# Kernel tuning notes

Measured on AMD Instinct MI355X. Metric: run time of the kernel, lower is better.

## Reference

```python
import jax, jax.numpy as jnp
import numpy as np

D_MODEL = 1024
N_HEADS = 16
HEAD_DIM = D_MODEL // N_HEADS


def apply_rope(x):
    # x: [B, S, H, Dh]; standard rotate-half RoPE over head_dim
    B, S, H, Dh = x.shape
    inv_freq = 1.0 / (10000.0 ** (jnp.arange(0, Dh, 2, dtype=jnp.float32) / Dh))  # [Dh/2]
    pos = jnp.arange(S, dtype=jnp.float32)
    freqs = pos[:, None] * inv_freq[None, :]          # [S, Dh/2]
    cos = jnp.cos(freqs)[None, :, None, :]            # [1, S, 1, Dh/2]
    sin = jnp.sin(freqs)[None, :, None, :]
    x1, x2 = x[..., :Dh // 2], x[..., Dh // 2:]
    return jnp.concatenate([x1 * cos - x2 * sin, x1 * sin + x2 * cos], axis=-1)


def setup_inputs() -> dict:
    key = jax.random.key(0)
    ks = jax.random.split(key, 8)
    B, S, D = 2, 2048, D_MODEL
    s = 0.02
    return {
        "query": jax.random.normal(ks[0], (B, S, D), dtype=jnp.float32),
        "key": jax.random.normal(ks[1], (B, S, D), dtype=jnp.float32),
        "value": jax.random.normal(ks[2], (B, S, D), dtype=jnp.float32),
        "Wq": jax.random.normal(ks[3], (D, D), dtype=jnp.float32) * s,
        "Wk": jax.random.normal(ks[4], (D, D), dtype=jnp.float32) * s,
        "Wv": jax.random.normal(ks[5], (D, D), dtype=jnp.float32) * s,
        "Wo": jax.random.normal(ks[6], (D, D), dtype=jnp.float32) * s,
        "bo": jax.random.normal(ks[7], (D,), dtype=jnp.float32) * s,
    }


def reference(query, key, value, Wq, Wk, Wv, Wo, bo):
    B, Sq, D = query.shape
    Skv = key.shape[1]
    H, Dh = N_HEADS, HEAD_DIM
    scale = Dh ** -0.5
    # projections (torch Linear: x @ W.T)
    q = (query @ Wq.T).reshape(B, Sq, H, Dh)
    k = (key @ Wk.T).reshape(B, Skv, H, Dh)
    v = (value @ Wv.T).reshape(B, Skv, H, Dh)
    q = apply_rope(q)
    k = apply_rope(k)
    # scores: [B, H, Sq, Skv]
    scores = jnp.einsum("bqhd,bkhd->bhqk", q, k) * scale
    attn_weights = jax.nn.softmax(scores, axis=-1)
    out = jnp.einsum("bhqk,bkhd->bqhd", attn_weights, v).reshape(B, Sq, D)
    out = out @ Wo.T + bo
    return out, attn_weights
```

## Files before the change

kernel.cpp:

```cpp
#include <hip/hip_runtime.h>
#include <math.h>

#define D_MODEL 1024
#define SEQ     2048
#define NB      2
#define NH      16
#define DH      64
#define ROWS    (NB*SEQ)
#define OUT_ELEMS ((size_t)ROWS*D_MODEL)

typedef short bf16x8 __attribute__((ext_vector_type(8)));
typedef short bf16x4 __attribute__((ext_vector_type(4)));
typedef float f32x4  __attribute__((ext_vector_type(4)));

#define AS1 __attribute__((address_space(1)))
#define AS3 __attribute__((address_space(3)))

__device__ __forceinline__ float bf2f(short u){
    union{float f; unsigned v;} x; x.v = ((unsigned)(unsigned short)u) << 16; return x.f;
}
__device__ __forceinline__ short f2bf(float f){
    union{float f; unsigned v;} x; x.f = f;
    unsigned r = (x.v + 0x7FFF + ((x.v >> 16) & 1)) >> 16;
    return (short)r;
}
__device__ __forceinline__ int swz8(int row, int slot){ return slot ^ ((row + (row>>3)) & 7); }

#define MFMA16(a,b,c) __builtin_amdgcn_mfma_f32_16x16x32_bf16((a),(b),(c),0,0,0)

#define EXPSC 0.18033688011112042f

__global__ __launch_bounds__(256) void prep(const float* __restrict__ Wq,
                                            const float* __restrict__ Wk,
                                            const float* __restrict__ Wv,
                                            const float* __restrict__ Wo,
                                            const float* __restrict__ qx,
                                            const float* __restrict__ kx,
                                            const float* __restrict__ vx,
                                            short* __restrict__ wqkv,
                                            short* __restrict__ wob,
                                            short* __restrict__ xb,
                                            float* __restrict__ tab)
{
    int i = blockIdx.x*256 + threadIdx.x;
    if (i < 1048576) {
        int sel = i >> 18;
        int loc = i & 262143;
        const float* src = sel==0 ? Wq : sel==1 ? Wk : sel==2 ? Wv : Wo;
        short* dst = sel < 3 ? wqkv + (size_t)sel*1048576 : wob;
        float4 v = *(const float4*)&src[(size_t)loc*4];
        bf16x4 o = { f2bf(v.x), f2bf(v.y), f2bf(v.z), f2bf(v.w) };
        *(bf16x4*)&dst[(size_t)loc*4] = o;
    } else if (i < 4194304) {
        int e = i - 1048576;
        int sel = e >> 20;
        int loc = e & 1048575;
        const float* src = sel==0 ? qx : sel==1 ? kx : vx;
        short* dst = xb + (size_t)sel*OUT_ELEMS;
        float4 v = *(const float4*)&src[(size_t)loc*4];
        bf16x4 o = { f2bf(v.x), f2bf(v.y), f2bf(v.z), f2bf(v.w) };
        *(bf16x4*)&dst[(size_t)loc*4] = o;
    } else {
        int e = i - 4194304;
        int j = e & 31, s = e >> 5;
        float ang = (float)s * exp2f(-(float)j * 0.41524101186092437f);
        float sn, cs; sincosf(ang, &sn, &cs);
        tab[(size_t)s*64 + j*2]     = cs;
        tab[(size_t)s*64 + j*2 + 1] = sn;
    }
}

__global__ __launch_bounds__(256) void gemm_qkv(const short* __restrict__ xb,
                                                const short* __restrict__ wqkv,
                                                const float* __restrict__ tab,
                                                short* __restrict__ qb,
                                                short* __restrict__ kb,
                                                short* __restrict__ vbt)
{
    const int z = blockIdx.z;
    const short* A = xb + (size_t)z*OUT_ELEMS;
    const short* B = wqkv + (size_t)z*D_MODEL*D_MODEL;

    __shared__ __align__(16) short Alds[128*64];
    __shared__ __align__(16) short Blds[128*64];
    const int t = threadIdx.x, lane = t & 63, wid = t >> 6;
    const int m0 = blockIdx.y << 7, n0 = blockIdx.x << 7;
    const int wm = (wid >> 1) << 6, wn = (wid & 1) << 6;
    const int l15 = lane & 15, l4 = lane >> 4;
    const int gchunk = (lane & 7) ^ (lane >> 3);
    const int rxor = l15 & 7;

    f32x4 acc[4][4] = {};

    for (int k0 = 0; k0 < D_MODEL; k0 += 64) {
        __syncthreads();
        #pragma unroll
        for (int u = 0; u < 4; ++u) {
            int row = u*32 + wid*8 + (lane >> 3);
            const short* ga = &A[(size_t)(m0 + row)*D_MODEL + k0 + gchunk*8];
            const short* gb = &B[(size_t)(n0 + row)*D_MODEL + k0 + gchunk*8];
            __builtin_amdgcn_global_load_lds((const AS1 unsigned*)ga,
                (AS3 unsigned*)&Alds[u*2048 + wid*512], 16, 0, 0);
            __builtin_amdgcn_global_load_lds((const AS1 unsigned*)gb,
                (AS3 unsigned*)&Blds[u*2048 + wid*512], 16, 0, 0);
        }
        __syncthreads();
        #pragma unroll
        for (int kk = 0; kk < 2; ++kk) {
            bf16x8 af[4], bfr[4];
            #pragma unroll
            for (int mf = 0; mf < 4; ++mf)
                af[mf] = *(const bf16x8*)&Alds[(wm + mf*16 + l15)*64
                                               + ((kk*4 + l4) ^ rxor)*8];
            #pragma unroll
            for (int nf = 0; nf < 4; ++nf)
                bfr[nf] = *(const bf16x8*)&Blds[(wn + nf*16 + l15)*64
                                                + ((kk*4 + l4) ^ rxor)*8];
            #pragma unroll
            for (int mf = 0; mf < 4; ++mf)
                #pragma unroll
                for (int nf = 0; nf < 4; ++nf)
                    acc[mf][nf] = MFMA16(af[mf], bfr[nf], acc[mf][nf]);
        }
    }

    if (z < 2) {
        short* C = z==0 ? qb : kb;
        #pragma unroll
        for (int mf = 0; mf < 4; ++mf)
            #pragma unroll
            for (int j = 0; j < 4; ++j) {
                int row = m0 + wm + mf*16 + l4*4 + j;
                int s = row & (SEQ-1);
                #pragma unroll
                for (int p = 0; p < 2; ++p) {
                    int d31 = p*16 + l15;
                    float2 cs2 = *(const float2*)&tab[(size_t)s*64 + d31*2];
                    float x1 = acc[mf][p][j], x2 = acc[mf][p+2][j];
                    size_t rb = (size_t)row*D_MODEL + n0 + wn;
                    C[rb + p*16 + l15]       = f2bf(x1*cs2.x - x2*cs2.y);
                    C[rb + (p+2)*16 + l15]   = f2bf(x1*cs2.y + x2*cs2.x);
                }
            }
    } else {
        #pragma unroll
        for (int nf = 0; nf < 4; ++nf) {
            int col = n0 + wn + nf*16 + l15;
            int hh = col >> 6, d = col & 63;
            #pragma unroll
            for (int mf = 0; mf < 4; ++mf)
                #pragma unroll
                for (int j = 0; j < 4; ++j) {
                    int row = m0 + wm + mf*16 + l4*4 + j;
                    int b = row >> 11, s = row & (SEQ-1);
                    vbt[(((size_t)(b*NH + hh))*DH + d)*SEQ + s] = f2bf(acc[mf][nf][j]);
                }
        }
    }
}

__global__ __launch_bounds__(256) void gemm_out(const short* __restrict__ A,
                                                const short* __restrict__ B,
                                                const float* __restrict__ bias,
                                                float* __restrict__ Cout)
{
    __shared__ __align__(16) short Alds[128*64];
    __shared__ __align__(16) short Blds[128*64];
    const int t = threadIdx.x, lane = t & 63, wid = t >> 6;
    const int m0 = blockIdx.y << 7, n0 = blockIdx.x << 7;
    const int wm = (wid >> 1) << 6, wn = (wid & 1) << 6;
    const int l15 = lane & 15, l4 = lane >> 4;
    const int gchunk = (lane & 7) ^ (lane >> 3);
    const int rxor = l15 & 7;

    f32x4 acc[4][4] = {};

    for (int k0 = 0; k0 < D_MODEL; k0 += 64) {
        __syncthreads();
        #pragma unroll
        for (int u = 0; u < 4; ++u) {
            int row = u*32 + wid*8 + (lane >> 3);
            const short* ga = &A[(size_t)(m0 + row)*D_MODEL + k0 + gchunk*8];
            const short* gb = &B[(size_t)(n0 + row)*D_MODEL + k0 + gchunk*8];
            __builtin_amdgcn_global_load_lds((const AS1 unsigned*)ga,
                (AS3 unsigned*)&Alds[u*2048 + wid*512], 16, 0, 0);
            __builtin_amdgcn_global_load_lds((const AS1 unsigned*)gb,
                (AS3 unsigned*)&Blds[u*2048 + wid*512], 16, 0, 0);
        }
        __syncthreads();
        #pragma unroll
        for (int kk = 0; kk < 2; ++kk) {
            bf16x8 af[4], bfr[4];
            #pragma unroll
            for (int mf = 0; mf < 4; ++mf)
                af[mf] = *(const bf16x8*)&Alds[(wm + mf*16 + l15)*64
                                               + ((kk*4 + l4) ^ rxor)*8];
            #pragma unroll
            for (int nf = 0; nf < 4; ++nf)
                bfr[nf] = *(const bf16x8*)&Blds[(wn + nf*16 + l15)*64
                                                + ((kk*4 + l4) ^ rxor)*8];
            #pragma unroll
            for (int mf = 0; mf < 4; ++mf)
                #pragma unroll
                for (int nf = 0; nf < 4; ++nf)
                    acc[mf][nf] = MFMA16(af[mf], bfr[nf], acc[mf][nf]);
        }
    }

    #pragma unroll
    for (int nf = 0; nf < 4; ++nf) {
        int col = n0 + wn + nf*16 + l15;
        float bv = bias[col];
        #pragma unroll
        for (int mf = 0; mf < 4; ++mf)
            #pragma unroll
            for (int j = 0; j < 4; ++j) {
                int row = m0 + wm + mf*16 + l4*4 + j;
                Cout[(size_t)row*D_MODEL + col] = acc[mf][nf][j] + bv;
            }
    }
}

__global__ __launch_bounds__(512) void attn_fused(const short* __restrict__ qb,
                                                  const short* __restrict__ kb,
                                                  const short* __restrict__ vbt,
                                                  float* __restrict__ attn,
                                                  short* __restrict__ aob)
{
    __shared__ __align__(16) short Klds[2][64*64];
    __shared__ __align__(16) short Vt  [2][64*64];
    __shared__ __align__(16) short Plds[8*16*64];
    const int t = threadIdx.x, lane = t & 63, wv = t >> 6;
    const int bid = blockIdx.x;
    const int nb = (bid & 7)*64 + (bid >> 3);
    const int rb = nb & 15, bh = nb >> 4;
    const int h = bh & 15;
    const size_t bs0 = (size_t)(bh >> 4) * SEQ;
    const int qrow0 = rb << 7;
    const int l15 = lane & 15, l4 = lane >> 4;
    const int srow = t >> 3, ssl = t & 7;
    const int soff = srow*64 + swz8(srow, ssl)*8;

    bf16x8 qf[2];
    {
        int qrow = qrow0 + wv*16 + l15;
        const short* qp = &qb[(bs0 + qrow)*D_MODEL + h*DH + l4*8];
        qf[0] = *(const bf16x8*)&qp[0];
        qf[1] = *(const bf16x8*)&qp[32];
    }

    const short* kbase  = &kb[(bs0 + srow)*D_MODEL + h*DH + ssl*8];
    const short* vtbase = &vbt[((size_t)bh*DH + srow)*SEQ + ssl*8];

    float lsum = 0.f;
    {
        bf16x8 kreg = *(const bf16x8*)&kbase[0];
        *(bf16x8*)&Klds[0][soff] = kreg;
        kreg = *(const bf16x8*)&kbase[(size_t)64*D_MODEL];
        __syncthreads();
        int cur = 0;
        for (int kt = 0; kt < SEQ; kt += 64, cur ^= 1) {
            if (kt + 64 < SEQ) {
                *(bf16x8*)&Klds[cur^1][soff] = kreg;
                if (kt + 128 < SEQ)
                    kreg = *(const bf16x8*)&kbase[(size_t)(kt+128)*D_MODEL];
            }
            f32x4 sc[4] = {};
            __builtin_amdgcn_s_setprio(1);
            #pragma unroll
            for (int kk = 0; kk < 2; ++kk)
                #pragma unroll
                for (int nf = 0; nf < 4; ++nf) {
                    int krow = nf*16 + l15;
                    bf16x8 kf = *(const bf16x8*)&Klds[cur][krow*64 + swz8(krow, kk*4 + l4)*8];
                    sc[nf] = MFMA16(kf, qf[kk], sc[nf]);
                }
            __builtin_amdgcn_s_setprio(0);
            #pragma unroll
            for (int nf = 0; nf < 4; ++nf)
                #pragma unroll
                for (int j = 0; j < 4; ++j)
                    lsum += exp2f(sc[nf][j]*EXPSC);
            __syncthreads();
        }
    }
    lsum += __shfl_xor(lsum, 16);
    lsum += __shfl_xor(lsum, 32);
    const float li = 1.0f / lsum;

    f32x4 o[4] = {};
    const size_t wrow = ((size_t)bh*SEQ + qrow0 + wv*16 + l15)*SEQ;
    short* pbase = &Plds[wv*1024 + l15*64];
    {
        bf16x8 kreg = *(const bf16x8*)&kbase[0];
        bf16x8 vreg = *(const bf16x8*)&vtbase[0];
        *(bf16x8*)&Klds[0][soff] = kreg;
        *(bf16x8*)&Vt  [0][soff] = vreg;
        kreg = *(const bf16x8*)&kbase[(size_t)64*D_MODEL];
        vreg = *(const bf16x8*)&vtbase[64];
        __syncthreads();
        int cur = 0;
        for (int kt = 0; kt < SEQ; kt += 64, cur ^= 1) {
            if (kt + 64 < SEQ) {
                *(bf16x8*)&Klds[cur^1][soff] = kreg;
                *(bf16x8*)&Vt  [cur^1][soff] = vreg;
                if (kt + 128 < SEQ) {
                    kreg = *(const bf16x8*)&kbase[(size_t)(kt+128)*D_MODEL];
                    vreg = *(const bf16x8*)&vtbase[kt+128];
                }
            }
            f32x4 sc[4] = {};
            __builtin_amdgcn_s_setprio(1);
            #pragma unroll
            for (int kk = 0; kk < 2; ++kk)
                #pragma unroll
                for (int nf = 0; nf < 4; ++nf) {
                    int krow = nf*16 + l15;
                    bf16x8 kf = *(const bf16x8*)&Klds[cur][krow*64 + swz8(krow, kk*4 + l4)*8];
                    sc[nf] = MFMA16(kf, qf[kk], sc[nf]);
                }
            __builtin_amdgcn_s_setprio(0);
            #pragma unroll
            for (int nf = 0; nf < 4; ++nf) {
                float w0 = exp2f(sc[nf][0]*EXPSC) * li;
                float w1 = exp2f(sc[nf][1]*EXPSC) * li;
                float w2 = exp2f(sc[nf][2]*EXPSC) * li;
                float w3 = exp2f(sc[nf][3]*EXPSC) * li;
                f32x4 wv4 = { w0, w1, w2, w3 };
                __builtin_nontemporal_store(wv4,
                    (f32x4*)&attn[wrow + kt + nf*16 + l4*4]);
                bf16x4 pw = { f2bf(w0), f2bf(w1), f2bf(w2), f2bf(w3) };
                *(bf16x4*)&pbase[swz8(l15, nf*2 + (l4>>1))*8 + (l4&1)*4] = pw;
            }
            __builtin_amdgcn_s_setprio(1);
            #pragma unroll
            for (int kk = 0; kk < 2; ++kk) {
                bf16x8 pa = *(const bf16x8*)&pbase[swz8(l15, kk*4 + l4)*8];
                #pragma unroll
                for (int nf = 0; nf < 4; ++nf) {
                    int d = nf*16 + l15;
                    bf16x8 vf = *(const bf16x8*)&Vt[cur][d*64 + swz8(d, kk*4 + l4)*8];
                    o[nf] = MFMA16(pa, vf, o[nf]);
                }
            }
            __builtin_amdgcn_s_setprio(0);
            __syncthreads();
        }
    }
    #pragma unroll
    for (int nf = 0; nf < 4; ++nf)
        #pragma unroll
        for (int j = 0; j < 4; ++j) {
            int qr = qrow0 + wv*16 + l4*4 + j;
            aob[(bs0 + qr)*D_MODEL + h*DH + nf*16 + l15] = f2bf(o[nf][j]);
        }
}

extern "C" void kernel_launch(void* const* d_in, const int* in_sizes, int n_in,
                              void* d_out, int out_size, void* d_ws, size_t ws_size,
                              hipStream_t stream)
{
    const float* query = (const float*)d_in[0];
    const float* key_  = (const float*)d_in[1];
    const float* value = (const float*)d_in[2];
    const float* Wq    = (const float*)d_in[3];
    const float* Wk    = (const float*)d_in[4];
    const float* Wv    = (const float*)d_in[5];
    const float* Wo    = (const float*)d_in[6];
    const float* bo    = (const float*)d_in[7];

    float* out  = (float*)d_out;
    float* attn = out + OUT_ELEMS;
    short* xb   = (short*)attn;

    short* wqkv = (short*)d_ws;
    short* wob  = wqkv + (size_t)3*1048576;
    short* qb   = wob  + (size_t)1048576;
    short* kb   = qb + OUT_ELEMS;
    short* vbt  = kb + OUT_ELEMS;
    short* aob  = vbt + OUT_ELEMS;
    float* tab  = (float*)(aob + OUT_ELEMS);

    dim3 blk(256);

    hipLaunchKernelGGL(prep, dim3(16640), blk, 0, stream,
                       Wq, Wk, Wv, Wo, query, key_, value, wqkv, wob, xb, tab);
    hipLaunchKernelGGL(gemm_qkv, dim3(8, 32, 3), blk, 0, stream,
                       xb, wqkv, tab, qb, kb, vbt);
    hipLaunchKernelGGL(attn_fused, dim3(512), dim3(512), 0, stream,
                       qb, kb, vbt, attn, aob);
    hipLaunchKernelGGL(gemm_out, dim3(8, 32), blk, 0, stream, aob, wob, bo, out);
}
```

Measured before the change: 291.8 us.

## Process two 16-row query subtiles per wave in attention with 256-thread blocks

The attention kernel now runs 4 waves of 256 threads instead of 8 waves, and each wave handles 32 query rows as two 16-row subtiles. Each K and V fragment read from LDS then feeds two MFMAs, halving LDS fragment reads per unit of work and giving each thread two tile rows to load. The cost is higher register pressure and fewer waves per block to hide the latency of the large attention-weight store stream.

Result: slower. 309.6 us (+6.1%).

```diff
diff --git a/kernel.cpp b/kernel.cpp
--- a/kernel.cpp
+++ b/kernel.cpp
@@ -221,7 +221,7 @@
     }
 }
 
-__global__ __launch_bounds__(512) void attn_fused(const short* __restrict__ qb,
+__global__ __launch_bounds__(256) void attn_fused(const short* __restrict__ qb,
                                                   const short* __restrict__ kb,
                                                   const short* __restrict__ vbt,
                                                   float* __restrict__ attn,
@@ -229,7 +229,7 @@
 {
     __shared__ __align__(16) short Klds[2][64*64];
     __shared__ __align__(16) short Vt  [2][64*64];
-    __shared__ __align__(16) short Plds[8*16*64];
+    __shared__ __align__(16) short Plds[4*2*16*64];
     const int t = threadIdx.x, lane = t & 63, wv = t >> 6;
     const int bid = blockIdx.x;
     const int nb = (bid & 7)*64 + (bid >> 3);
@@ -238,34 +238,44 @@
     const size_t bs0 = (size_t)(bh >> 4) * SEQ;
     const int qrow0 = rb << 7;
     const int l15 = lane & 15, l4 = lane >> 4;
-    const int srow = t >> 3, ssl = t & 7;
-    const int soff = srow*64 + swz8(srow, ssl)*8;
-
-    bf16x8 qf[2];
+    const int sr0 = t >> 3, ssl = t & 7;
+    const int soff0 = sr0*64 + swz8(sr0, ssl)*8;
+    const int soff1 = (sr0+32)*64 + swz8(sr0+32, ssl)*8;
+
+    bf16x8 qf[2][2];
+    #pragma unroll
+    for (int sub = 0; sub < 2; ++sub) {
+        int qrow = qrow0 + wv*32 + sub*16 + l15;
+        const short* qp = &qb[(bs0 + qrow)*D_MODEL + h*DH + l4*8];
+        qf[sub][0] = *(const bf16x8*)&qp[0];
+        qf[sub][1] = *(const bf16x8*)&qp[32];
+    }
+
+    const short* kbase0  = &kb[(bs0 + sr0)*D_MODEL + h*DH + ssl*8];
+    const short* kbase1  = &kb[(bs0 + sr0 + 32)*D_MODEL + h*DH + ssl*8];
+    const short* vtbase0 = &vbt[((size_t)bh*DH + sr0)*SEQ + ssl*8];
+    const short* vtbase1 = &vbt[((size_t)bh*DH + sr0 + 32)*SEQ + ssl*8];
+
+    float lsum0 = 0.f, lsum1 = 0.f;
     {
-        int qrow = qrow0 + wv*16 + l15;
-        const short* qp = &qb[(bs0 + qrow)*D_MODEL + h*DH + l4*8];
-        qf[0] = *(const bf16x8*)&qp[0];
-        qf[1] = *(const bf16x8*)&qp[32];
-    }
-
-    const short* kbase  = &kb[(bs0 + srow)*D_MODEL + h*DH + ssl*8];
-    const short* vtbase = &vbt[((size_t)bh*DH + srow)*SEQ + ssl*8];
-
-    float lsum = 0.f;
-    {
-        bf16x8 kreg = *(const bf16x8*)&kbase[0];
-        *(bf16x8*)&Klds[0][soff] = kreg;
-        kreg = *(const bf16x8*)&kbase[(size_t)64*D_MODEL];
+        bf16x8 kr0 = *(const bf16x8*)&kbase0[0];
+        bf16x8 kr1 = *(const bf16x8*)&kbase1[0];
+        *(bf16x8*)&Klds[0][soff0] = kr0;
+        *(bf16x8*)&Klds[0][soff1] = kr1;
+        kr0 = *(const bf16x8*)&kbase0[(size_t)64*D_MODEL];
+        kr1 = *(const bf16x8*)&kbase1[(size_t)64*D_MODEL];
         __syncthreads();
         int cur = 0;
         for (int kt = 0; kt < SEQ; kt += 64, cur ^= 1) {
             if (kt + 64 < SEQ) {
-                *(bf16x8*)&Klds[cur^1][soff] = kreg;
-                if (kt + 128 < SEQ)
-                    kreg = *(const bf16x8*)&kbase[(size_t)(kt+128)*D_MODEL];
-            }
-            f32x4 sc[4] = {};
+                *(bf16x8*)&Klds[cur^1][soff0] = kr0;
+                *(bf16x8*)&Klds[cur^1][soff1] = kr1;
+                if (kt + 128 < SEQ) {
+                    kr0 = *(const bf16x8*)&kbase0[(size_t)(kt+128)*D_MODEL];
+                    kr1 = *(const bf16x8*)&kbase1[(size_t)(kt+128)*D_MODEL];
+                }
+            }
+            f32x4 sc0[4] = {}, sc1[4] = {};
             __builtin_amdgcn_s_setprio(1);
             #pragma unroll
             for (int kk = 0; kk < 2; ++kk)
@@ -273,43 +283,61 @@
                 for (int nf = 0; nf < 4; ++nf) {
                     int krow = nf*16 + l15;
                     bf16x8 kf = *(const bf16x8*)&Klds[cur][krow*64 + swz8(krow, kk*4 + l4)*8];
-                    sc[nf] = MFMA16(kf, qf[kk], sc[nf]);
+                    sc0[nf] = MFMA16(kf, qf[0][kk], sc0[nf]);
+                    sc1[nf] = MFMA16(kf, qf[1][kk], sc1[nf]);
                 }
             __builtin_amdgcn_s_setprio(0);
             #pragma unroll
             for (int nf = 0; nf < 4; ++nf)
                 #pragma unroll
-                for (int j = 0; j < 4; ++j)
-                    lsum += exp2f(sc[nf][j]*EXPSC);
+                for (int j = 0; j < 4; ++j) {
+                    lsum0 += exp2f(sc0[nf][j]*EXPSC);
+                    lsum1 += exp2f(sc1[nf][j]*EXPSC);
+                }
             __syncthreads();
         }
     }
-    lsum += __shfl_xor(lsum, 16);
-    lsum += __shfl_xor(lsum, 32);
-    const float li = 1.0f / lsum;
-
-    f32x4 o[4] = {};
-    const size_t wrow = ((size_t)bh*SEQ + qrow0 + wv*16 + l15)*SEQ;
-    short* pbase = &Plds[wv*1024 + l15*64];
+    lsum0 += __shfl_xor(lsum0, 16);
+    lsum0 += __shfl_xor(lsum0, 32);
+    lsum1 += __shfl_xor(lsum1, 16);
+    lsum1 += __shfl_xor(lsum1, 32);
+    const float li0 = 1.0f / lsum0;
+    const float li1 = 1.0f / lsum1;
+
+    f32x4 o0[4] = {}, o1[4] = {};
+    const size_t wrow0 = ((size_t)bh*SEQ + qrow0 + wv*32 + l15)*SEQ;
+    const size_t wrow1 = wrow0 + (size_t)16*SEQ;
+    short* pb0 = &Plds[(wv*2 + 0)*1024 + l15*64];
+    short* pb1 = &Plds[(wv*2 + 1)*1024 + l15*64];
     {
-        bf16x8 kreg = *(const bf16x8*)&kbase[0];
-        bf16x8 vreg = *(const bf16x8*)&vtbase[0];
-        *(bf16x8*)&Klds[0][soff] = kreg;
-        *(bf16x8*)&Vt  [0][soff] = vreg;
-        kreg = *(const bf16x8*)&kbase[(size_t)64*D_MODEL];
-        vreg = *(const bf16x8*)&vtbase[64];
+        bf16x8 kr0 = *(const bf16x8*)&kbase0[0];
+        bf16x8 kr1 = *(const bf16x8*)&kbase1[0];
+        bf16x8 vr0 = *(const bf16x8*)&vtbase0[0];
+        bf16x8 vr1 = *(const bf16x8*)&vtbase1[0];
+        *(bf16x8*)&Klds[0][soff0] = kr0;
+        *(bf16x8*)&Klds[0][soff1] = kr1;
+        *(bf16x8*)&Vt  [0][soff0] = vr0;
+        *(bf16x8*)&Vt  [0][soff1] = vr1;
+        kr0 = *(const bf16x8*)&kbase0[(size_t)64*D_MODEL];
+        kr1 = *(const bf16x8*)&kbase1[(size_t)64*D_MODEL];
+        vr0 = *(const bf16x8*)&vtbase0[64];
+        vr1 = *(const bf16x8*)&vtbase1[64];
         __syncthreads();
         int cur = 0;
         for (int kt = 0; kt < SEQ; kt += 64, cur ^= 1) {
             if (kt + 64 < SEQ) {
-                *(bf16x8*)&Klds[cur^1][soff] = kreg;
-                *(bf16x8*)&Vt  [cur^1][soff] = vreg;
+                *(bf16x8*)&Klds[cur^1][soff0] = kr0;
+                *(bf16x8*)&Klds[cur^1][soff1] = kr1;
+                *(bf16x8*)&Vt  [cur^1][soff0] = vr0;
+                *(bf16x8*)&Vt  [cur^1][soff1] = vr1;
                 if (kt + 128 < SEQ) {
-                    kreg = *(const bf16x8*)&kbase[(size_t)(kt+128)*D_MODEL];
-                    vreg = *(const bf16x8*)&vtbase[kt+128];
-                }
-            }
-            f32x4 sc[4] = {};
+                    kr0 = *(const bf16x8*)&kbase0[(size_t)(kt+128)*D_MODEL];
+                    kr1 = *(const bf16x8*)&kbase1[(size_t)(kt+128)*D_MODEL];
+                    vr0 = *(const bf16x8*)&vtbase0[kt+128];
+                    vr1 = *(const bf16x8*)&vtbase1[kt+128];
+                }
+            }
+            f32x4 sc0[4] = {}, sc1[4] = {};
             __builtin_amdgcn_s_setprio(1);
             #pragma unroll
             for (int kk = 0; kk < 2; ++kk)
@@ -317,30 +345,45 @@
                 for (int nf = 0; nf < 4; ++nf) {
                     int krow = nf*16 + l15;
                     bf16x8 kf = *(const bf16x8*)&Klds[cur][krow*64 + swz8(krow, kk*4 + l4)*8];
-                    sc[nf] = MFMA16(kf, qf[kk], sc[nf]);
+                    sc0[nf] = MFMA16(kf, qf[0][kk], sc0[nf]);
+                    sc1[nf] = MFMA16(kf, qf[1][kk], sc1[nf]);
                 }
             __builtin_amdgcn_s_setprio(0);
             #pragma unroll
             for (int nf = 0; nf < 4; ++nf) {
-                float w0 = exp2f(sc[nf][0]*EXPSC) * li;
-                float w1 = exp2f(sc[nf][1]*EXPSC) * li;
-                float w2 = exp2f(sc[nf][2]*EXPSC) * li;
-                float w3 = exp2f(sc[nf][3]*EXPSC) * li;
+                float w0 = exp2f(sc0[nf][0]*EXPSC) * li0;
+                float w1 = exp2f(sc0[nf][1]*EXPSC) * li0;
+                float w2 = exp2f(sc0[nf][2]*EXPSC) * li0;
+                float w3 = exp2f(sc0[nf][3]*EXPSC) * li0;
                 f32x4 wv4 = { w0, w1, w2, w3 };
                 __builtin_nontemporal_store(wv4,
-                    (f32x4*)&attn[wrow + kt + nf*16 + l4*4]);
+                    (f32x4*)&attn[wrow0 + kt + nf*16 + l4*4]);
                 bf16x4 pw = { f2bf(w0), f2bf(w1), f2bf(w2), f2bf(w3) };
-                *(bf16x4*)&pbase[swz8(l15, nf*2 + (l4>>1))*8 + (l4&1)*4] = pw;
+                *(bf16x4*)&pb0[swz8(l15, nf*2 + (l4>>1))*8 + (l4&1)*4] = pw;
+            }
+            #pragma unroll
+            for (int nf = 0; nf < 4; ++nf) {
+                float w0 = exp2f(sc1[nf][0]*EXPSC) * li1;
+                float w1 = exp2f(sc1[nf][1]*EXPSC) * li1;
+                float w2 = exp2f(sc1[nf][2]*EXPSC) * li1;
+                float w3 = exp2f(sc1[nf][3]*EXPSC) * li1;
+                f32x4 wv4 = { w0, w1, w2, w3 };
+                __builtin_nontemporal_store(wv4,
+                    (f32x4*)&attn[wrow1 + kt + nf*16 + l4*4]);
+                bf16x4 pw = { f2bf(w0), f2bf(w1), f2bf(w2), f2bf(w3) };
+                *(bf16x4*)&pb1[swz8(l15, nf*2 + (l4>>1))*8 + (l4&1)*4] = pw;
             }
             __builtin_amdgcn_s_setprio(1);
             #pragma unroll
             for (int kk = 0; kk < 2; ++kk) {
-                bf16x8 pa = *(const bf16x8*)&pbase[swz8(l15, kk*4 + l4)*8];
+                bf16x8 pa0 = *(const bf16x8*)&pb0[swz8(l15, kk*4 + l4)*8];
+                bf16x8 pa1 = *(const bf16x8*)&pb1[swz8(l15, kk*4 + l4)*8];
                 #pragma unroll
                 for (int nf = 0; nf < 4; ++nf) {
                     int d = nf*16 + l15;
                     bf16x8 vf = *(const bf16x8*)&Vt[cur][d*64 + swz8(d, kk*4 + l4)*8];
-                    o[nf] = MFMA16(pa, vf, o[nf]);
+                    o0[nf] = MFMA16(pa0, vf, o0[nf]);
+                    o1[nf] = MFMA16(pa1, vf, o1[nf]);
                 }
             }
             __builtin_amdgcn_s_setprio(0);
@@ -351,8 +394,9 @@
     for (int nf = 0; nf < 4; ++nf)
         #pragma unroll
         for (int j = 0; j < 4; ++j) {
-            int qr = qrow0 + wv*16 + l4*4 + j;
-            aob[(bs0 + qr)*D_MODEL + h*DH + nf*16 + l15] = f2bf(o[nf][j]);
+            int qr0 = qrow0 + wv*32 + l4*4 + j;
+            aob[(bs0 + qr0)*D_MODEL + h*DH + nf*16 + l15]      = f2bf(o0[nf][j]);
+            aob[(bs0 + qr0 + 16)*D_MODEL + h*DH + nf*16 + l15] = f2bf(o1[nf][j]);
         }
 }
 
@@ -387,7 +431,7 @@
                        Wq, Wk, Wv, Wo, query, key_, value, wqkv, wob, xb, tab);
     hipLaunchKernelGGL(gemm_qkv, dim3(8, 32, 3), blk, 0, stream,
                        xb, wqkv, tab, qb, kb, vbt);
-    hipLaunchKernelGGL(attn_fused, dim3(512), dim3(512), 0, stream,
+    hipLaunchKernelGGL(attn_fused, dim3(512), blk, 0, stream,
                        qb, kb, vbt, attn, aob);
     hipLaunchKernelGGL(gemm_out, dim3(8, 32), blk, 0, stream, aob, wob, bo, out);
 }
```
